# Optimization experiments

Measured on AMD Instinct MI355X. Metric: run time of the kernel, lower is better.

The kernel has to match this reference:

```python
import jax, jax.numpy as jnp
import numpy as np

B, S_IMG, S_TXT, D, H, HD = 1, 4096, 512, 3072, 24, 128
EPS = 1e-5
SCALE = 1.0 / np.sqrt(HD)


def _linear(x, W, b=None):
    # torch nn.Linear: y = x @ W.T + b, W is [out, in]
    y = jnp.einsum('bsd,od->bso', x, W)
    return y if b is None else y + b


def _rmsnorm(x, w):
    # over last dim (head_dim), torch nn.RMSNorm with affine weight
    var = jnp.mean(jnp.square(x), axis=-1, keepdims=True)
    return x * jax.lax.rsqrt(var + EPS) * w


def _rope(x, cos, sin):
    # x: [B, S, H, D]; cos/sin: [S, D]; interleaved-pair rotation
    xr = x.reshape(*x.shape[:-1], HD // 2, 2)
    x_real, x_imag = xr[..., 0], xr[..., 1]
    x_rot = jnp.stack([-x_imag, x_real], axis=-1).reshape(x.shape)
    return x * cos[None, :, None, :] + x_rot * sin[None, :, None, :]


def setup_inputs() -> dict:
    key = jax.random.key(0)
    ks = jax.random.split(key, 24)
    s = 0.02
    inp = {
        'hidden_states': jax.random.normal(ks[0], (B, S_IMG, D), jnp.float32),
        'encoder_hidden_states': jax.random.normal(ks[1], (B, S_TXT, D), jnp.float32),
        'rope_cos': jax.random.uniform(ks[2], (S_IMG + S_TXT, HD), jnp.float32),
        'rope_sin': jax.random.uniform(ks[3], (S_IMG + S_TXT, HD), jnp.float32),
        # image-stream qkv (bias=False)
        'Wq': jax.random.normal(ks[4], (D, D), jnp.float32) * s,
        'Wk': jax.random.normal(ks[5], (D, D), jnp.float32) * s,
        'Wv': jax.random.normal(ks[6], (D, D), jnp.float32) * s,
        # text-stream qkv (bias=True)
        'Waq': jax.random.normal(ks[7], (D, D), jnp.float32) * s,
        'baq': jnp.zeros((D,), jnp.float32),
        'Wak': jax.random.normal(ks[8], (D, D), jnp.float32) * s,
        'bak': jnp.zeros((D,), jnp.float32),
        'Wav': jax.random.normal(ks[9], (D, D), jnp.float32) * s,
        'bav': jnp.zeros((D,), jnp.float32),
        # output projections (bias=True)
        'Wo': jax.random.normal(ks[10], (D, D), jnp.float32) * s,
        'bo': jnp.zeros((D,), jnp.float32),
        'Wao': jax.random.normal(ks[11], (D, D), jnp.float32) * s,
        'bao': jnp.zeros((D,), jnp.float32),
        # RMSNorm weights on head_dim
        'wq_norm': jnp.ones((HD,), jnp.float32),
        'wk_norm': jnp.ones((HD,), jnp.float32),
        'waq_norm': jnp.ones((HD,), jnp.float32),
        'wak_norm': jnp.ones((HD,), jnp.float32),
    }
    return inp


def reference(hidden_states, encoder_hidden_states, rope_cos, rope_sin,
              Wq, Wk, Wv, Waq, baq, Wak, bak, Wav, bav,
              Wo, bo, Wao, bao, wq_norm, wk_norm, waq_norm, wak_norm):
    # image-stream qkv -> [B, S_img, H, HD]
    q = _linear(hidden_states, Wq).reshape(B, S_IMG, H, HD)
    k = _linear(hidden_states, Wk).reshape(B, S_IMG, H, HD)
    v = _linear(hidden_states, Wv).reshape(B, S_IMG, H, HD)
    q = _rmsnorm(q, wq_norm)
    k = _rmsnorm(k, wk_norm)
    # text-stream qkv -> [B, S_txt, H, HD]
    eq = _linear(encoder_hidden_states, Waq, baq).reshape(B, S_TXT, H, HD)
    ek = _linear(encoder_hidden_states, Wak, bak).reshape(B, S_TXT, H, HD)
    ev = _linear(encoder_hidden_states, Wav, bav).reshape(B, S_TXT, H, HD)
    eq = _rmsnorm(eq, waq_norm)
    ek = _rmsnorm(ek, wak_norm)
    # concat [encoder, image] along sequence
    q = jnp.concatenate([eq, q], axis=1)  # [B, S_total, H, HD]
    k = jnp.concatenate([ek, k], axis=1)
    v = jnp.concatenate([ev, v], axis=1)
    # RoPE on joint sequence
    q = _rope(q, rope_cos, rope_sin)
    k = _rope(k, rope_cos, rope_sin)
    # SDPA over joint sequence
    scores = jnp.einsum('bqhd,bkhd->bhqk', q, k) * SCALE
    probs = jax.nn.softmax(scores, axis=-1)
    out = jnp.einsum('bhqk,bkhd->bqhd', probs, v)  # [B, S_total, H, HD]
    out = out.reshape(B, S_IMG + S_TXT, D)
    enc_out = _linear(out[:, :S_TXT], Wao, bao)
    img_out = _linear(out[:, S_TXT:], Wo, bo)
    return (img_out, enc_out)
```

## Files before the change

kernel.cpp:

```cpp
#include <hip/hip_runtime.h>

typedef __bf16 bf16_t;
typedef __bf16 bf16x8 __attribute__((ext_vector_type(8)));
typedef float  f32x4  __attribute__((ext_vector_type(4)));

#define S_IMG 4096
#define S_TXT 512
#define S_TOT 4608
#define DMODEL 3072
#define NH 24
#define HD 128

__device__ __forceinline__ void load_lds16(const void* g, void* l) {
  __builtin_amdgcn_global_load_lds(
      (const __attribute__((address_space(1))) void*)g,
      (__attribute__((address_space(3))) void*)l, 16, 0, 0);
}

#define BARRIER() do { asm volatile("" ::: "memory");                          \
                       __builtin_amdgcn_s_barrier();                           \
                       asm volatile("" ::: "memory"); } while (0)

__global__ __launch_bounds__(256) void f2b_kernel(const float* __restrict__ in,
                                                  bf16_t* __restrict__ out, int n) {
  int i = (blockIdx.x * 256 + threadIdx.x) * 4;
  if (i >= n) return;
  float4 v = *(const float4*)(in + i);
  union { bf16_t b[4]; uint2 u; } pk;
  pk.b[0] = (bf16_t)v.x; pk.b[1] = (bf16_t)v.y;
  pk.b[2] = (bf16_t)v.z; pk.b[3] = (bf16_t)v.w;
  *(uint2*)(out + i) = pk.u;
}

__global__ __launch_bounds__(256) void f2b2_kernel(
    const float* __restrict__ in0, bf16_t* __restrict__ out0,
    const float* __restrict__ in1, bf16_t* __restrict__ out1, int nb) {
  int b = blockIdx.x;
  const float* in = (b < nb) ? in0 : in1;
  bf16_t* out = (b < nb) ? out0 : out1;
  int i = (((b < nb) ? b : b - nb) * 256 + threadIdx.x) * 4;
  float4 v = *(const float4*)(in + i);
  union { bf16_t b[4]; uint2 u; } pk;
  pk.b[0] = (bf16_t)v.x; pk.b[1] = (bf16_t)v.y;
  pk.b[2] = (bf16_t)v.z; pk.b[3] = (bf16_t)v.w;
  *(uint2*)(out + i) = pk.u;
}

template <typename OT>
__global__ __launch_bounds__(512, 2) void gemm256(
    const bf16_t* __restrict__ A0, const bf16_t* __restrict__ B0,
    OT* __restrict__ C0, const float* __restrict__ bias0, int mt0,
    const bf16_t* __restrict__ A1, const bf16_t* __restrict__ B1,
    OT* __restrict__ C1, const float* __restrict__ bias1, int swzq)
{
  const int NT = DMODEL / 64;
  __shared__ bf16_t As[2][2][256 * 32];
  __shared__ bf16_t Bs[2][2][256 * 32];

  int bid = blockIdx.x;
  int t = (bid & 7) * swzq + (bid >> 3);
  int nb0 = mt0 * 12;
  const bf16_t* A; const bf16_t* B; OT* C; const float* bias;
  if (t < nb0) { A = A0; B = B0; C = C0; bias = bias0; }
  else { t -= nb0; A = A1; B = B1; C = C1; bias = bias1; }
  int bx = t % 12, by = t / 12;

  int tid = threadIdx.x;
  int lane = tid & 63, wid = tid >> 6;
  int l15 = lane & 15, lg = lane >> 4;
  int wm = wid >> 2, wn = wid & 3;
  int sx = (lg ^ ((l15 >> 1) & 3)) * 8;

  const bf16_t* Ag = A + (size_t)by * 256 * DMODEL;
  const bf16_t* Bg = B + (size_t)bx * 256 * DMODEL;

  int ur0 = tid >> 2;
  int uc0 = ((tid & 3) ^ ((tid >> 3) & 3)) * 8;

  auto stage = [&](int ht) {
    int T = ht >> 2, sl = ht & 3, kh = sl >> 1;
    const bf16_t* G = (sl & 1) ? Bg : Ag;
    bf16_t* L = (sl & 1) ? &Bs[T & 1][kh][0] : &As[T & 1][kh][0];
    int kbase = T * 64 + kh * 32;
    #pragma unroll
    for (int j = 0; j < 2; j++) {
      int r = j * 128 + ur0;
      load_lds16(G + (size_t)r * DMODEL + kbase + uc0,
                 (char*)L + (size_t)(j * 512 + tid) * 16);
    }
  };

  f32x4 acc[8][4];
  f32x4 zero = {0.f, 0.f, 0.f, 0.f};
  #pragma unroll
  for (int m = 0; m < 8; m++)
    #pragma unroll
    for (int n = 0; n < 4; n++) acc[m][n] = zero;

  stage(0); stage(1); stage(2); stage(3); stage(4); stage(5);
  asm volatile("s_waitcnt vmcnt(8)" ::: "memory");
  BARRIER();

  for (int T = 0; T < NT; ++T) {
    int cur = T & 1;
    const bf16_t* A0s = &As[cur][0][0];
    const bf16_t* A1s = &As[cur][1][0];
    const bf16_t* B0s = &Bs[cur][0][0];
    const bf16_t* B1s = &Bs[cur][1][0];
    bf16x8 af[4], bfr[4];

    #pragma unroll
    for (int n = 0; n < 4; n++)
      bfr[n] = *(const bf16x8*)(B0s + (wn * 64 + n * 16 + l15) * 32 + sx);
    #pragma unroll
    for (int m = 0; m < 4; m++)
      af[m] = *(const bf16x8*)(A0s + (wm * 128 + m * 16 + l15) * 32 + sx);
    if (T + 1 < NT) stage(4 * T + 6);
    BARRIER();
    __builtin_amdgcn_s_setprio(1);
    #pragma unroll
    for (int m = 0; m < 4; m++)
      #pragma unroll
      for (int n = 0; n < 4; n++)
        acc[m][n] = __builtin_amdgcn_mfma_f32_16x16x32_bf16(af[m], bfr[n], acc[m][n], 0, 0, 0);
    __builtin_amdgcn_s_setprio(0);
    BARRIER();

    #pragma unroll
    for (int m = 0; m < 4; m++)
      af[m] = *(const bf16x8*)(A0s + (wm * 128 + 64 + m * 16 + l15) * 32 + sx);
    if (T + 1 < NT) stage(4 * T + 7);
    BARRIER();
    __builtin_amdgcn_s_setprio(1);
    #pragma unroll
    for (int m = 0; m < 4; m++)
      #pragma unroll
      for (int n = 0; n < 4; n++)
        acc[4 + m][n] = __builtin_amdgcn_mfma_f32_16x16x32_bf16(af[m], bfr[n], acc[4 + m][n], 0, 0, 0);
    __builtin_amdgcn_s_setprio(0);
    if (T < NT - 1) asm volatile("s_waitcnt vmcnt(8)" ::: "memory");
    else            asm volatile("s_waitcnt vmcnt(0)" ::: "memory");
    BARRIER();

    #pragma unroll
    for (int n = 0; n < 4; n++)
      bfr[n] = *(const bf16x8*)(B1s + (wn * 64 + n * 16 + l15) * 32 + sx);
    #pragma unroll
    for (int m = 0; m < 4; m++)
      af[m] = *(const bf16x8*)(A1s + (wm * 128 + m * 16 + l15) * 32 + sx);
    if (T + 2 < NT) stage(4 * T + 8);
    BARRIER();
    __builtin_amdgcn_s_setprio(1);
    #pragma unroll
    for (int m = 0; m < 4; m++)
      #pragma unroll
      for (int n = 0; n < 4; n++)
        acc[m][n] = __builtin_amdgcn_mfma_f32_16x16x32_bf16(af[m], bfr[n], acc[m][n], 0, 0, 0);
    __builtin_amdgcn_s_setprio(0);
    BARRIER();

    #pragma unroll
    for (int m = 0; m < 4; m++)
      af[m] = *(const bf16x8*)(A1s + (wm * 128 + 64 + m * 16 + l15) * 32 + sx);
    if (T + 2 < NT) stage(4 * T + 9);
    BARRIER();
    __builtin_amdgcn_s_setprio(1);
    #pragma unroll
    for (int m = 0; m < 4; m++)
      #pragma unroll
      for (int n = 0; n < 4; n++)
        acc[4 + m][n] = __builtin_amdgcn_mfma_f32_16x16x32_bf16(af[m], bfr[n], acc[4 + m][n], 0, 0, 0);
    __builtin_amdgcn_s_setprio(0);
    if (T < NT - 2)       asm volatile("s_waitcnt vmcnt(8)" ::: "memory");
    else if (T == NT - 2) asm volatile("s_waitcnt vmcnt(4)" ::: "memory");
    BARRIER();
  }

  size_t row0 = (size_t)by * 256 + wm * 128;
  int col0 = bx * 256 + wn * 64;
  #pragma unroll
  for (int n = 0; n < 4; n++) {
    int col = col0 + n * 16 + l15;
    float bv = bias ? bias[col] : 0.f;
    #pragma unroll
    for (int m = 0; m < 8; m++) {
      #pragma unroll
      for (int r = 0; r < 4; r++) {
        size_t row = row0 + m * 16 + lg * 4 + r;
        C[row * DMODEL + col] = (OT)(acc[m][n][r] + bv);
      }
    }
  }
}

__global__ __launch_bounds__(256) void qk_post(
    const bf16_t* __restrict__ qbuf, const bf16_t* __restrict__ kbuf,
    const float* __restrict__ cosb, const float* __restrict__ sinb,
    const float* __restrict__ wqn, const float* __restrict__ wkn,
    const float* __restrict__ waqn, const float* __restrict__ wakn,
    bf16_t* __restrict__ Qh, bf16_t* __restrict__ Kh)
{
  int gw = blockIdx.x * 4 + (threadIdx.x >> 6);
  int lane = threadIdx.x & 63;
  int s = gw / NH, h = gw - (gw / NH) * NH;
  if (s >= S_TOT) return;
  int d0 = lane * 2;
  const bf16_t* qp = qbuf + (size_t)s * DMODEL + h * HD + d0;
  const bf16_t* kp = kbuf + (size_t)s * DMODEL + h * HD + d0;
  float q0 = (float)qp[0], q1 = (float)qp[1];
  float k0 = (float)kp[0], k1 = (float)kp[1];
  float sq = q0 * q0 + q1 * q1, sk = k0 * k0 + k1 * k1;
  #pragma unroll
  for (int m = 1; m < 64; m <<= 1) { sq += __shfl_xor(sq, m); sk += __shfl_xor(sk, m); }
  float rq = rsqrtf(sq * (1.f / HD) + 1e-5f);
  float rk = rsqrtf(sk * (1.f / HD) + 1e-5f);
  const float* qn = (s < S_TXT) ? waqn : wqn;
  const float* kn = (s < S_TXT) ? wakn : wkn;
  q0 *= rq * qn[d0]; q1 *= rq * qn[d0 + 1];
  k0 *= rk * kn[d0]; k1 *= rk * kn[d0 + 1];
  float c0 = cosb[s * HD + d0], c1 = cosb[s * HD + d0 + 1];
  float s0 = sinb[s * HD + d0], s1 = sinb[s * HD + d0 + 1];
  const float SCALE = 0.1275174319942397f;
  float oq0 = (q0 * c0 - q1 * s0) * SCALE;
  float oq1 = (q1 * c1 + q0 * s1) * SCALE;
  float ok0 = k0 * c0 - k1 * s0;
  float ok1 = k1 * c1 + k0 * s1;
  size_t ob = ((size_t)h * S_TOT + s) * HD + d0;
  union { bf16_t b[2]; unsigned int u; } pq, pk;
  pq.b[0] = (bf16_t)oq0; pq.b[1] = (bf16_t)oq1;
  pk.b[0] = (bf16_t)ok0; pk.b[1] = (bf16_t)ok1;
  *(unsigned int*)(Qh + ob) = pq.u;
  *(unsigned int*)(Kh + ob) = pk.u;
}

__global__ __launch_bounds__(256) void v_trans(const bf16_t* __restrict__ vbuf,
                                               bf16_t* __restrict__ Vt) {
  __shared__ bf16_t tile[64 * 130];
  int h = blockIdx.y, s0 = blockIdx.x * 64;
  int tid = threadIdx.x;
  #pragma unroll
  for (int i = 0; i < 16; i++) {
    int idx = tid + i * 256;
    int sr = idx >> 6, dp = idx & 63;
    unsigned int u = *(const unsigned int*)(vbuf + (size_t)(s0 + sr) * DMODEL + h * HD + dp * 2);
    *(unsigned int*)&tile[sr * 130 + dp * 2] = u;
  }
  __syncthreads();
  #pragma unroll
  for (int i = 0; i < 16; i++) {
    int idx = tid + i * 256;
    int d = idx >> 5, scp = idx & 31;
    union { bf16_t b[2]; unsigned int u; } pk;
    pk.b[0] = tile[(scp * 2) * 130 + d];
    pk.b[1] = tile[(scp * 2 + 1) * 130 + d];
    *(unsigned int*)(Vt + ((size_t)h * HD + d) * S_TOT + s0 + scp * 2) = pk.u;
  }
}

__global__ __launch_bounds__(256, 2) void attn_kernel(
    const bf16_t* __restrict__ Qh, const bf16_t* __restrict__ Kh,
    const bf16_t* __restrict__ Vt, bf16_t* __restrict__ O)
{
  int bid = blockIdx.x;
  int orig = (bid & 7) * 108 + (bid >> 3);
  int h = orig / 36;
  int q0 = (orig % 36) * 128;

  int tid = threadIdx.x, w = tid >> 6, lane = tid & 63;
  int l15 = lane & 15, lg = lane >> 4;
  int sw = (l15 & 7) << 4;

  __shared__ bf16_t Ks[2][64 * 128];
  __shared__ bf16_t Vs[2][128 * 64];
  __shared__ bf16_t Ps[4][32 * 64];

  const bf16_t* Kbase = Kh + (size_t)h * S_TOT * HD;
  const bf16_t* Vbase = Vt + (size_t)h * HD * S_TOT;
  bf16_t* Pw = &Ps[w][0];

  bf16x8 qf[2][4];
  #pragma unroll
  for (int qh = 0; qh < 2; qh++) {
    const bf16_t* Qrow = Qh + ((size_t)h * S_TOT + q0 + w * 32 + qh * 16 + l15) * HD + lg * 8;
    #pragma unroll
    for (int dc = 0; dc < 4; dc++) qf[qh][dc] = *(const bf16x8*)(Qrow + dc * 32);
  }

  f32x4 o[2][8];
  f32x4 zero = {0.f, 0.f, 0.f, 0.f};
  #pragma unroll
  for (int qh = 0; qh < 2; qh++)
    #pragma unroll
    for (int i = 0; i < 8; i++) o[qh][i] = zero;
  float m0 = -1e30f, m1 = -1e30f, l0 = 0.f, l1 = 0.f;

#define STAGE(buf, kt) do {                                                    \
    _Pragma("unroll")                                                          \
    for (int i_ = 0; i_ < 4; i_++) {                    \
      int Lb = (tid + i_ * 256) * 16; int row = Lb >> 8, cb = Lb & 255;        \
      int sb = cb ^ ((row & 7) << 4);                                          \
      load_lds16(Kbase + (size_t)((kt) + row) * HD + (sb >> 1),                \
                 (char*)Ks[buf] + Lb);                                         \
    }                                                                          \
    _Pragma("unroll")                                                          \
    for (int i_ = 0; i_ < 4; i_++) {                   \
      int Lb = (tid + i_ * 256) * 16; int row = Lb >> 7, cb = Lb & 127;        \
      int sb = cb ^ ((row & 7) << 4);                                          \
      load_lds16(Vbase + (size_t)row * S_TOT + (kt) + (sb >> 1),               \
                 (char*)Vs[buf] + Lb);                                         \
    }                                                                          \
  } while (0)

#define BODY(CUR) do {                                                         \
    f32x4 sacc[2][4];                                                          \
    _Pragma("unroll")                                                          \
    for (int qh = 0; qh < 2; qh++)                                             \
      _Pragma("unroll")                                                        \
      for (int c = 0; c < 4; c++) sacc[qh][c] = zero;                          \
    const char* Kc = (const char*)Ks[CUR];                                     \
    _Pragma("unroll")                                                          \
    for (int c = 0; c < 4; c++) {                                              \
      int row = c * 16 + l15;                                                  \
      int rs = (row & 7) << 4;                                                 \
      const char* kr = Kc + row * 256;                                         \
      _Pragma("unroll")                                                        \
      for (int dc = 0; dc < 4; dc++) {                                         \
        bf16x8 kf = *(const bf16x8*)(kr + ((dc * 64 + lg * 16) ^ rs));         \
        sacc[0][c] = __builtin_amdgcn_mfma_f32_16x16x32_bf16(kf, qf[0][dc], sacc[0][c], 0, 0, 0); \
        sacc[1][c] = __builtin_amdgcn_mfma_f32_16x16x32_bf16(kf, qf[1][dc], sacc[1][c], 0, 0, 0); \
      }                                                                        \
    }                                                                          \
    float px0 = sacc[0][0][0], px1 = sacc[1][0][0];                            \
    _Pragma("unroll")                                                          \
    for (int c = 0; c < 4; c++)                                                \
      _Pragma("unroll")                                                        \
      for (int r = 0; r < 4; r++) {                                            \
        px0 = fmaxf(px0, sacc[0][c][r]);                                       \
        px1 = fmaxf(px1, sacc[1][c][r]);                                       \
      }                                                                        \
    px0 = fmaxf(px0, __shfl_xor(px0, 16)); px0 = fmaxf(px0, __shfl_xor(px0, 32)); \
    px1 = fmaxf(px1, __shfl_xor(px1, 16)); px1 = fmaxf(px1, __shfl_xor(px1, 32)); \
    bool need = (px0 > m0 + 8.f) || (px1 > m1 + 8.f);                          \
    if (__any(need)) {                                                         \
      float mn0 = fmaxf(m0, px0), mn1 = fmaxf(m1, px1);                        \
      float a0 = exp2f(m0 - mn0), a1 = exp2f(m1 - mn1);                        \
      m0 = mn0; m1 = mn1; l0 *= a0; l1 *= a1;                                  \
      _Pragma("unroll")                                                        \
      for (int r = 0; r < 4; r++) {                                            \
        float f0 = __shfl(a0, lg * 4 + r);                                     \
        float f1 = __shfl(a1, lg * 4 + r);                                     \
        _Pragma("unroll")                                                      \
        for (int dn = 0; dn < 8; dn++) { o[0][dn][r] *= f0; o[1][dn][r] *= f1; } \
      }                                                                        \
    }                                                                          \
    _Pragma("unroll")                                                          \
    for (int qh = 0; qh < 2; qh++) {                                           \
      float m = qh ? m1 : m0;                                                  \
      float rsum = 0.f;                                                        \
      char* Prow = (char*)Pw + (qh * 16 + l15) * 128;                          \
      _Pragma("unroll")                                                        \
      for (int c = 0; c < 4; c++) {                                            \
        union { bf16_t b[4]; uint2 u; } pk;                                    \
        _Pragma("unroll")                                                      \
        for (int r = 0; r < 4; r++) {                                          \
          float p = exp2f(sacc[qh][c][r] - m);                                 \
          rsum += p;                                                           \
          pk.b[r] = (bf16_t)p;                                                 \
        }                                                                      \
        *(uint2*)(Prow + ((c * 32 + lg * 8) ^ sw)) = pk.u;                     \
      }                                                                        \
      rsum += __shfl_xor(rsum, 16);                                            \
      rsum += __shfl_xor(rsum, 32);                                            \
      if (qh) l1 += rsum; else l0 += rsum;                                     \
    }                                                                          \
    bf16x8 pf[2][2];                                                           \
    _Pragma("unroll")                                                          \
    for (int qh = 0; qh < 2; qh++) {                                           \
      const char* Prow = (const char*)Pw + (qh * 16 + l15) * 128;              \
      _Pragma("unroll")                                                        \
      for (int kc = 0; kc < 2; kc++)                                           \
        pf[qh][kc] = *(const bf16x8*)(Prow + ((kc * 64 + lg * 16) ^ sw));      \
    }                                                                          \
    const char* Vc = (const char*)Vs[CUR];                                     \
    _Pragma("unroll")                                                          \
    for (int dn = 0; dn < 8; dn++) {                                           \
      int row = dn * 16 + l15;                                                 \
      int rs2 = (row & 7) << 4;                                                \
      const char* vr = Vc + row * 128;                                         \
      bf16x8 vf0 = *(const bf16x8*)(vr + ((lg * 16) ^ rs2));                   \
      bf16x8 vf1 = *(const bf16x8*)(vr + ((64 + lg * 16) ^ rs2));              \
      o[0][dn] = __builtin_amdgcn_mfma_f32_16x16x32_bf16(pf[0][0], vf0, o[0][dn], 0, 0, 0); \
      o[0][dn] = __builtin_amdgcn_mfma_f32_16x16x32_bf16(pf[0][1], vf1, o[0][dn], 0, 0, 0); \
      o[1][dn] = __builtin_amdgcn_mfma_f32_16x16x32_bf16(pf[1][0], vf0, o[1][dn], 0, 0, 0); \
      o[1][dn] = __builtin_amdgcn_mfma_f32_16x16x32_bf16(pf[1][1], vf1, o[1][dn], 0, 0, 0); \
    }                                                                          \
  } while (0)

  STAGE(0, 0);
  __syncthreads();

  const int NT = S_TOT / 64;
  for (int tt = 0; tt < NT; tt += 2) {
    STAGE(1, (tt + 1) * 64);
    BODY(0);
    __syncthreads();
    if (tt + 2 < NT) STAGE(0, (tt + 2) * 64);
    BODY(1);
    __syncthreads();
  }
#undef BODY
#undef STAGE

  #pragma unroll
  for (int qh = 0; qh < 2; qh++) {
    #pragma unroll
    for (int r = 0; r < 4; r++) {
      float lv = __shfl(qh ? l1 : l0, lg * 4 + r);
      float inv = 1.f / lv;
      size_t srow = (size_t)q0 + w * 32 + qh * 16 + lg * 4 + r;
      #pragma unroll
      for (int dn = 0; dn < 8; dn++)
        O[srow * DMODEL + h * HD + dn * 16 + l15] = (bf16_t)(o[qh][dn][r] * inv);
    }
  }
}

extern "C" void kernel_launch(void* const* d_in, const int* in_sizes, int n_in,
                              void* d_out, int out_size, void* d_ws, size_t ws_size,
                              hipStream_t stream) {
  const float* hidden = (const float*)d_in[0];
  const float* enc    = (const float*)d_in[1];
  const float* ropec  = (const float*)d_in[2];
  const float* ropes  = (const float*)d_in[3];
  const float* Wq  = (const float*)d_in[4];
  const float* Wk  = (const float*)d_in[5];
  const float* Wv  = (const float*)d_in[6];
  const float* Waq = (const float*)d_in[7];
  const float* baq = (const float*)d_in[8];
  const float* Wak = (const float*)d_in[9];
  const float* bak = (const float*)d_in[10];
  const float* Wav = (const float*)d_in[11];
  const float* bav = (const float*)d_in[12];
  const float* Wo  = (const float*)d_in[13];
  const float* bo  = (const float*)d_in[14];
  const float* Wao = (const float*)d_in[15];
  const float* bao = (const float*)d_in[16];
  const float* wqn = (const float*)d_in[17];
  const float* wkn = (const float*)d_in[18];
  const float* waqn = (const float*)d_in[19];
  const float* wakn = (const float*)d_in[20];

  const size_t WSZ = (size_t)DMODEL * DMODEL;
  const size_t SEQSZ = (size_t)S_TOT * DMODEL;
  if (ws_size < (2 * WSZ + 6 * SEQSZ) * sizeof(bf16_t)) return;

  bf16_t* s0   = (bf16_t*)d_ws;
  bf16_t* s1   = s0 + WSZ;
  bf16_t* xbi  = s1 + WSZ;
  bf16_t* xbt  = xbi + (size_t)S_IMG * DMODEL;
  bf16_t* qbuf = xbi + SEQSZ;
  bf16_t* kbuf = qbuf + SEQSZ;
  bf16_t* vbuf = kbuf + SEQSZ;
  bf16_t* Kh   = vbuf + SEQSZ;
  bf16_t* Vh   = Kh + SEQSZ;
  bf16_t* Qh   = xbi;
  bf16_t* attn_o = qbuf;
  float* outf = (float*)d_out;

  f2b_kernel<<<S_IMG * DMODEL / 1024, 256, 0, stream>>>(hidden, xbi, S_IMG * DMODEL);
  f2b_kernel<<<S_TXT * DMODEL / 1024, 256, 0, stream>>>(enc, xbt, S_TXT * DMODEL);

  const int WB = (int)(WSZ / 1024);
  f2b2_kernel<<<2 * WB, 256, 0, stream>>>(Wq, s0, Waq, s1, WB);
  gemm256<bf16_t><<<216, 512, 0, stream>>>(
      xbi, s0, qbuf + (size_t)S_TXT * DMODEL, nullptr, 16,
      xbt, s1, qbuf, baq, 27);
  f2b2_kernel<<<2 * WB, 256, 0, stream>>>(Wk, s0, Wak, s1, WB);
  gemm256<bf16_t><<<216, 512, 0, stream>>>(
      xbi, s0, kbuf + (size_t)S_TXT * DMODEL, nullptr, 16,
      xbt, s1, kbuf, bak, 27);
  f2b2_kernel<<<2 * WB, 256, 0, stream>>>(Wv, s0, Wav, s1, WB);
  gemm256<bf16_t><<<216, 512, 0, stream>>>(
      xbi, s0, vbuf + (size_t)S_TXT * DMODEL, nullptr, 16,
      xbt, s1, vbuf, bav, 27);

  qk_post<<<S_TOT * NH / 4, 256, 0, stream>>>(qbuf, kbuf, ropec, ropes,
                                              wqn, wkn, waqn, wakn, Qh, Kh);
  v_trans<<<dim3(S_TOT / 64, NH), 256, 0, stream>>>(vbuf, Vh);

  attn_kernel<<<36 * 24, 256, 0, stream>>>(Qh, Kh, Vh, attn_o);

  f2b2_kernel<<<2 * WB, 256, 0, stream>>>(Wo, s0, Wao, s1, WB);
  gemm256<float><<<216, 512, 0, stream>>>(
      attn_o + (size_t)S_TXT * DMODEL, s0, outf, bo, 16,
      attn_o, s1, outf + (size_t)S_IMG * DMODEL, bao, 27);
}
```

Baseline: 968.5 us.

## Fuse Q/K/V projections into one GEMM launch and pipeline attention K/V loads

Converts all three QKV weight pairs to bf16 up front, placing them in scratch regions (the Kh buffer and the output buffer), and runs a single 648-block GEMM that computes Q, K and V together by treating the weights as a wide N dimension. The output column block picks which matrix to write. Text-stream biases move out of the GEMM and into qk_post and v_trans, with V's bias now added after bf16 rounding. The attention loop is reworked to keep two K/V tiles in flight, using explicit vmcnt waits and raw barriers in place of __syncthreads, and raises wave priority around the MFMA blocks. These changes aim to cut launch count and tail effects and to overlap global loads with compute, at the cost of reusing buffers that the later code must not still need.

```diff
diff --git a/kernel.cpp b/kernel.cpp
--- a/kernel.cpp
+++ b/kernel.cpp
@@ -51,7 +51,8 @@
     const bf16_t* __restrict__ A0, const bf16_t* __restrict__ B0,
     OT* __restrict__ C0, const float* __restrict__ bias0, int mt0,
     const bf16_t* __restrict__ A1, const bf16_t* __restrict__ B1,
-    OT* __restrict__ C1, const float* __restrict__ bias1, int swzq)
+    OT* __restrict__ C1, const float* __restrict__ bias1,
+    int nbt, size_t matStride, int swzq)
 {
   const int NT = DMODEL / 64;
   __shared__ bf16_t As[2][2][256 * 32];
@@ -59,11 +60,12 @@
 
   int bid = blockIdx.x;
   int t = (bid & 7) * swzq + (bid >> 3);
-  int nb0 = mt0 * 12;
+  int nb0 = mt0 * nbt;
   const bf16_t* A; const bf16_t* B; OT* C; const float* bias;
   if (t < nb0) { A = A0; B = B0; C = C0; bias = bias0; }
   else { t -= nb0; A = A1; B = B1; C = C1; bias = bias1; }
-  int bx = t % 12, by = t / 12;
+  int bx = t % nbt, by = t / nbt;
+  int mat = bx / 12;
 
   int tid = threadIdx.x;
   int lane = tid & 63, wid = tid >> 6;
@@ -176,8 +178,9 @@
     BARRIER();
   }
 
+  OT* Cm = C + (size_t)mat * matStride;
   size_t row0 = (size_t)by * 256 + wm * 128;
-  int col0 = bx * 256 + wn * 64;
+  int col0 = (bx % 12) * 256 + wn * 64;
   #pragma unroll
   for (int n = 0; n < 4; n++) {
     int col = col0 + n * 16 + l15;
@@ -187,7 +190,7 @@
       #pragma unroll
       for (int r = 0; r < 4; r++) {
         size_t row = row0 + m * 16 + lg * 4 + r;
-        C[row * DMODEL + col] = (OT)(acc[m][n][r] + bv);
+        Cm[row * DMODEL + col] = (OT)(acc[m][n][r] + bv);
       }
     }
   }
@@ -198,6 +201,7 @@
     const float* __restrict__ cosb, const float* __restrict__ sinb,
     const float* __restrict__ wqn, const float* __restrict__ wkn,
     const float* __restrict__ waqn, const float* __restrict__ wakn,
+    const float* __restrict__ baq, const float* __restrict__ bak,
     bf16_t* __restrict__ Qh, bf16_t* __restrict__ Kh)
 {
   int gw = blockIdx.x * 4 + (threadIdx.x >> 6);
@@ -209,6 +213,10 @@
   const bf16_t* kp = kbuf + (size_t)s * DMODEL + h * HD + d0;
   float q0 = (float)qp[0], q1 = (float)qp[1];
   float k0 = (float)kp[0], k1 = (float)kp[1];
+  if (s < S_TXT) {
+    q0 += baq[h * HD + d0]; q1 += baq[h * HD + d0 + 1];
+    k0 += bak[h * HD + d0]; k1 += bak[h * HD + d0 + 1];
+  }
   float sq = q0 * q0 + q1 * q1, sk = k0 * k0 + k1 * k1;
   #pragma unroll
   for (int m = 1; m < 64; m <<= 1) { sq += __shfl_xor(sq, m); sk += __shfl_xor(sk, m); }
@@ -234,16 +242,23 @@
 }
 
 __global__ __launch_bounds__(256) void v_trans(const bf16_t* __restrict__ vbuf,
+                                               const float* __restrict__ bav,
                                                bf16_t* __restrict__ Vt) {
   __shared__ bf16_t tile[64 * 130];
   int h = blockIdx.y, s0 = blockIdx.x * 64;
   int tid = threadIdx.x;
+  bool txt = (s0 < S_TXT);
   #pragma unroll
   for (int i = 0; i < 16; i++) {
     int idx = tid + i * 256;
     int sr = idx >> 6, dp = idx & 63;
-    unsigned int u = *(const unsigned int*)(vbuf + (size_t)(s0 + sr) * DMODEL + h * HD + dp * 2);
-    *(unsigned int*)&tile[sr * 130 + dp * 2] = u;
+    union { bf16_t b[2]; unsigned int u; } pk;
+    pk.u = *(const unsigned int*)(vbuf + (size_t)(s0 + sr) * DMODEL + h * HD + dp * 2);
+    if (txt) {
+      pk.b[0] = (bf16_t)((float)pk.b[0] + bav[h * HD + dp * 2]);
+      pk.b[1] = (bf16_t)((float)pk.b[1] + bav[h * HD + dp * 2 + 1]);
+    }
+    *(unsigned int*)&tile[sr * 130 + dp * 2] = pk.u;
   }
   __syncthreads();
   #pragma unroll
@@ -318,6 +333,7 @@
       _Pragma("unroll")                                                        \
       for (int c = 0; c < 4; c++) sacc[qh][c] = zero;                          \
     const char* Kc = (const char*)Ks[CUR];                                     \
+    __builtin_amdgcn_s_setprio(1);                                             \
     _Pragma("unroll")                                                          \
     for (int c = 0; c < 4; c++) {                                              \
       int row = c * 16 + l15;                                                  \
@@ -330,6 +346,7 @@
         sacc[1][c] = __builtin_amdgcn_mfma_f32_16x16x32_bf16(kf, qf[1][dc], sacc[1][c], 0, 0, 0); \
       }                                                                        \
     }                                                                          \
+    __builtin_amdgcn_s_setprio(0);                                             \
     float px0 = sacc[0][0][0], px1 = sacc[1][0][0];                            \
     _Pragma("unroll")                                                          \
     for (int c = 0; c < 4; c++)                                                \
@@ -382,6 +399,7 @@
         pf[qh][kc] = *(const bf16x8*)(Prow + ((kc * 64 + lg * 16) ^ sw));      \
     }                                                                          \
     const char* Vc = (const char*)Vs[CUR];                                     \
+    __builtin_amdgcn_s_setprio(1);                                             \
     _Pragma("unroll")                                                          \
     for (int dn = 0; dn < 8; dn++) {                                           \
       int row = dn * 16 + l15;                                                 \
@@ -394,19 +412,25 @@
       o[1][dn] = __builtin_amdgcn_mfma_f32_16x16x32_bf16(pf[1][0], vf0, o[1][dn], 0, 0, 0); \
       o[1][dn] = __builtin_amdgcn_mfma_f32_16x16x32_bf16(pf[1][1], vf1, o[1][dn], 0, 0, 0); \
     }                                                                          \
+    __builtin_amdgcn_s_setprio(0);                                             \
   } while (0)
 
   STAGE(0, 0);
-  __syncthreads();
+  STAGE(1, 64);
 
   const int NT = S_TOT / 64;
   for (int tt = 0; tt < NT; tt += 2) {
-    STAGE(1, (tt + 1) * 64);
+    asm volatile("s_waitcnt vmcnt(8)" ::: "memory");
+    BARRIER();
     BODY(0);
-    __syncthreads();
+    BARRIER();
     if (tt + 2 < NT) STAGE(0, (tt + 2) * 64);
+    if (tt + 2 < NT) asm volatile("s_waitcnt vmcnt(8)" ::: "memory");
+    else             asm volatile("s_waitcnt vmcnt(0)" ::: "memory");
+    BARRIER();
     BODY(1);
-    __syncthreads();
+    BARRIER();
+    if (tt + 3 < NT) STAGE(1, (tt + 3) * 64);
   }
 #undef BODY
 #undef STAGE
@@ -465,33 +489,30 @@
   bf16_t* Vh   = Kh + SEQSZ;
   bf16_t* Qh   = xbi;
   bf16_t* attn_o = qbuf;
+  bf16_t* wimg = Kh;
+  bf16_t* wtxt = (bf16_t*)d_out;
   float* outf = (float*)d_out;
 
   f2b_kernel<<<S_IMG * DMODEL / 1024, 256, 0, stream>>>(hidden, xbi, S_IMG * DMODEL);
   f2b_kernel<<<S_TXT * DMODEL / 1024, 256, 0, stream>>>(enc, xbt, S_TXT * DMODEL);
 
   const int WB = (int)(WSZ / 1024);
-  f2b2_kernel<<<2 * WB, 256, 0, stream>>>(Wq, s0, Waq, s1, WB);
-  gemm256<bf16_t><<<216, 512, 0, stream>>>(
-      xbi, s0, qbuf + (size_t)S_TXT * DMODEL, nullptr, 16,
-      xbt, s1, qbuf, baq, 27);
-  f2b2_kernel<<<2 * WB, 256, 0, stream>>>(Wk, s0, Wak, s1, WB);
-  gemm256<bf16_t><<<216, 512, 0, stream>>>(
-      xbi, s0, kbuf + (size_t)S_TXT * DMODEL, nullptr, 16,
-      xbt, s1, kbuf, bak, 27);
-  f2b2_kernel<<<2 * WB, 256, 0, stream>>>(Wv, s0, Wav, s1, WB);
-  gemm256<bf16_t><<<216, 512, 0, stream>>>(
-      xbi, s0, vbuf + (size_t)S_TXT * DMODEL, nullptr, 16,
-      xbt, s1, vbuf, bav, 27);
+  f2b2_kernel<<<2 * WB, 256, 0, stream>>>(Wq, wimg,           Waq, wtxt,           WB);
+  f2b2_kernel<<<2 * WB, 256, 0, stream>>>(Wk, wimg + WSZ,     Wak, wtxt + WSZ,     WB);
+  f2b2_kernel<<<2 * WB, 256, 0, stream>>>(Wv, wimg + 2 * WSZ, Wav, wtxt + 2 * WSZ, WB);
+
+  gemm256<bf16_t><<<648, 512, 0, stream>>>(
+      xbi, wimg, qbuf + (size_t)S_TXT * DMODEL, nullptr, 16,
+      xbt, wtxt, qbuf, nullptr, 36, SEQSZ, 81);
 
   qk_post<<<S_TOT * NH / 4, 256, 0, stream>>>(qbuf, kbuf, ropec, ropes,
-                                              wqn, wkn, waqn, wakn, Qh, Kh);
-  v_trans<<<dim3(S_TOT / 64, NH), 256, 0, stream>>>(vbuf, Vh);
+                                              wqn, wkn, waqn, wakn, baq, bak, Qh, Kh);
+  v_trans<<<dim3(S_TOT / 64, NH), 256, 0, stream>>>(vbuf, bav, Vh);
 
   attn_kernel<<<36 * 24, 256, 0, stream>>>(Qh, Kh, Vh, attn_o);
 
   f2b2_kernel<<<2 * WB, 256, 0, stream>>>(Wo, s0, Wao, s1, WB);
   gemm256<float><<<216, 512, 0, stream>>>(
       attn_o + (size_t)S_TXT * DMODEL, s0, outf, bo, 16,
-      attn_o, s1, outf + (size_t)S_IMG * DMODEL, bao, 27);
-}
+      attn_o, s1, outf + (size_t)S_IMG * DMODEL, bao, 12, 0, 27);
+}
```

New measurement: 1.044 ms. 1.08x slower.

## Split attention block across 8 waves with 16 query rows each

Applied to the files above, without the earlier changes.

Doubles the attention block to 512 threads, with each of 8 waves owning 16 query rows instead of each of 4 waves owning 32. K/V tiles are still shared in LDS but staged by twice as many threads, and per-wave register state (Q fragments, output accumulators, softmax stats) is halved. The aim is more wave-level parallelism and latency hiding with lower register pressure. In exchange, each K/V LDS fragment read now feeds half as many MFMAs, so LDS traffic per flop rises and barrier costs are shared by more waves.

```diff
diff --git a/kernel.cpp b/kernel.cpp
--- a/kernel.cpp
+++ b/kernel.cpp
@@ -257,7 +257,7 @@
   }
 }
 
-__global__ __launch_bounds__(256, 2) void attn_kernel(
+__global__ __launch_bounds__(512, 2) void attn_kernel(
     const bf16_t* __restrict__ Qh, const bf16_t* __restrict__ Kh,
     const bf16_t* __restrict__ Vt, bf16_t* __restrict__ O)
 {
@@ -272,39 +272,36 @@
 
   __shared__ bf16_t Ks[2][64 * 128];
   __shared__ bf16_t Vs[2][128 * 64];
-  __shared__ bf16_t Ps[4][32 * 64];
+  __shared__ bf16_t Ps[8][16 * 64];
 
   const bf16_t* Kbase = Kh + (size_t)h * S_TOT * HD;
   const bf16_t* Vbase = Vt + (size_t)h * HD * S_TOT;
   bf16_t* Pw = &Ps[w][0];
 
-  bf16x8 qf[2][4];
-  #pragma unroll
-  for (int qh = 0; qh < 2; qh++) {
-    const bf16_t* Qrow = Qh + ((size_t)h * S_TOT + q0 + w * 32 + qh * 16 + l15) * HD + lg * 8;
-    #pragma unroll
-    for (int dc = 0; dc < 4; dc++) qf[qh][dc] = *(const bf16x8*)(Qrow + dc * 32);
-  }
-
-  f32x4 o[2][8];
+  bf16x8 qf[4];
+  {
+    const bf16_t* Qrow = Qh + ((size_t)h * S_TOT + q0 + w * 16 + l15) * HD + lg * 8;
+    #pragma unroll
+    for (int dc = 0; dc < 4; dc++) qf[dc] = *(const bf16x8*)(Qrow + dc * 32);
+  }
+
+  f32x4 o[8];
   f32x4 zero = {0.f, 0.f, 0.f, 0.f};
   #pragma unroll
-  for (int qh = 0; qh < 2; qh++)
-    #pragma unroll
-    for (int i = 0; i < 8; i++) o[qh][i] = zero;
-  float m0 = -1e30f, m1 = -1e30f, l0 = 0.f, l1 = 0.f;
+  for (int i = 0; i < 8; i++) o[i] = zero;
+  float m0 = -1e30f, l0 = 0.f;
 
 #define STAGE(buf, kt) do {                                                    \
     _Pragma("unroll")                                                          \
-    for (int i_ = 0; i_ < 4; i_++) {                    \
-      int Lb = (tid + i_ * 256) * 16; int row = Lb >> 8, cb = Lb & 255;        \
+    for (int i_ = 0; i_ < 2; i_++) {           \
+      int Lb = (tid + i_ * 512) * 16; int row = Lb >> 8, cb = Lb & 255;        \
       int sb = cb ^ ((row & 7) << 4);                                          \
       load_lds16(Kbase + (size_t)((kt) + row) * HD + (sb >> 1),                \
                  (char*)Ks[buf] + Lb);                                         \
     }                                                                          \
     _Pragma("unroll")                                                          \
-    for (int i_ = 0; i_ < 4; i_++) {                   \
-      int Lb = (tid + i_ * 256) * 16; int row = Lb >> 7, cb = Lb & 127;        \
+    for (int i_ = 0; i_ < 2; i_++) {                   \
+      int Lb = (tid + i_ * 512) * 16; int row = Lb >> 7, cb = Lb & 127;        \
       int sb = cb ^ ((row & 7) << 4);                                          \
       load_lds16(Vbase + (size_t)row * S_TOT + (kt) + (sb >> 1),               \
                  (char*)Vs[buf] + Lb);                                         \
@@ -312,11 +309,8 @@
   } while (0)
 
 #define BODY(CUR) do {                                                         \
-    f32x4 sacc[2][4];                                                          \
-    _Pragma("unroll")                                                          \
-    for (int qh = 0; qh < 2; qh++)                                             \
-      _Pragma("unroll")                                                        \
-      for (int c = 0; c < 4; c++) sacc[qh][c] = zero;                          \
+    f32x4 sacc[4];                                                             \
+    sacc[0] = zero; sacc[1] = zero; sacc[2] = zero; sacc[3] = zero;            \
     const char* Kc = (const char*)Ks[CUR];                                     \
     _Pragma("unroll")                                                          \
     for (int c = 0; c < 4; c++) {                                              \
@@ -326,44 +320,36 @@
       _Pragma("unroll")                                                        \
       for (int dc = 0; dc < 4; dc++) {                                         \
         bf16x8 kf = *(const bf16x8*)(kr + ((dc * 64 + lg * 16) ^ rs));         \
-        sacc[0][c] = __builtin_amdgcn_mfma_f32_16x16x32_bf16(kf, qf[0][dc], sacc[0][c], 0, 0, 0); \
-        sacc[1][c] = __builtin_amdgcn_mfma_f32_16x16x32_bf16(kf, qf[1][dc], sacc[1][c], 0, 0, 0); \
+        sacc[c] = __builtin_amdgcn_mfma_f32_16x16x32_bf16(kf, qf[dc], sacc[c], 0, 0, 0); \
       }                                                                        \
     }                                                                          \
-    float px0 = sacc[0][0][0], px1 = sacc[1][0][0];                            \
+    float px = sacc[0][0];                                                     \
     _Pragma("unroll")                                                          \
     for (int c = 0; c < 4; c++)                                                \
       _Pragma("unroll")                                                        \
-      for (int r = 0; r < 4; r++) {                                            \
-        px0 = fmaxf(px0, sacc[0][c][r]);                                       \
-        px1 = fmaxf(px1, sacc[1][c][r]);                                       \
-      }                                                                        \
-    px0 = fmaxf(px0, __shfl_xor(px0, 16)); px0 = fmaxf(px0, __shfl_xor(px0, 32)); \
-    px1 = fmaxf(px1, __shfl_xor(px1, 16)); px1 = fmaxf(px1, __shfl_xor(px1, 32)); \
-    bool need = (px0 > m0 + 8.f) || (px1 > m1 + 8.f);                          \
-    if (__any(need)) {                                                         \
-      float mn0 = fmaxf(m0, px0), mn1 = fmaxf(m1, px1);                        \
-      float a0 = exp2f(m0 - mn0), a1 = exp2f(m1 - mn1);                        \
-      m0 = mn0; m1 = mn1; l0 *= a0; l1 *= a1;                                  \
+      for (int r = 0; r < 4; r++) px = fmaxf(px, sacc[c][r]);                  \
+    px = fmaxf(px, __shfl_xor(px, 16));                                        \
+    px = fmaxf(px, __shfl_xor(px, 32));                                        \
+    if (__any(px > m0 + 8.f)) {                                                \
+      float mn0 = fmaxf(m0, px);                                               \
+      float a0 = exp2f(m0 - mn0);                                              \
+      m0 = mn0; l0 *= a0;                                                      \
       _Pragma("unroll")                                                        \
       for (int r = 0; r < 4; r++) {                                            \
         float f0 = __shfl(a0, lg * 4 + r);                                     \
-        float f1 = __shfl(a1, lg * 4 + r);                                     \
         _Pragma("unroll")                                                      \
-        for (int dn = 0; dn < 8; dn++) { o[0][dn][r] *= f0; o[1][dn][r] *= f1; } \
+        for (int dn = 0; dn < 8; dn++) o[dn][r] *= f0;                         \
       }                                                                        \
     }                                                                          \
-    _Pragma("unroll")                                                          \
-    for (int qh = 0; qh < 2; qh++) {                                           \
-      float m = qh ? m1 : m0;                                                  \
+    {                                                                          \
       float rsum = 0.f;                                                        \
-      char* Prow = (char*)Pw + (qh * 16 + l15) * 128;                          \
+      char* Prow = (char*)Pw + l15 * 128;                                      \
       _Pragma("unroll")                                                        \
       for (int c = 0; c < 4; c++) {                                            \
         union { bf16_t b[4]; uint2 u; } pk;                                    \
         _Pragma("unroll")                                                      \
         for (int r = 0; r < 4; r++) {                                          \
-          float p = exp2f(sacc[qh][c][r] - m);                                 \
+          float p = exp2f(sacc[c][r] - m0);                                    \
           rsum += p;                                                           \
           pk.b[r] = (bf16_t)p;                                                 \
         }                                                                      \
@@ -371,15 +357,14 @@
       }                                                                        \
       rsum += __shfl_xor(rsum, 16);                                            \
       rsum += __shfl_xor(rsum, 32);                                            \
-      if (qh) l1 += rsum; else l0 += rsum;                                     \
-    }                                                                          \
-    bf16x8 pf[2][2];                                                           \
-    _Pragma("unroll")                                                          \
-    for (int qh = 0; qh < 2; qh++) {                                           \
-      const char* Prow = (const char*)Pw + (qh * 16 + l15) * 128;              \
+      l0 += rsum;                                                              \
+    }                                                                          \
+    bf16x8 pf[2];                                                              \
+    {                                                                          \
+      const char* Prow = (const char*)Pw + l15 * 128;                          \
       _Pragma("unroll")                                                        \
       for (int kc = 0; kc < 2; kc++)                                           \
-        pf[qh][kc] = *(const bf16x8*)(Prow + ((kc * 64 + lg * 16) ^ sw));      \
+        pf[kc] = *(const bf16x8*)(Prow + ((kc * 64 + lg * 16) ^ sw));          \
     }                                                                          \
     const char* Vc = (const char*)Vs[CUR];                                     \
     _Pragma("unroll")                                                          \
@@ -389,10 +374,8 @@
       const char* vr = Vc + row * 128;                                         \
       bf16x8 vf0 = *(const bf16x8*)(vr + ((lg * 16) ^ rs2));                   \
       bf16x8 vf1 = *(const bf16x8*)(vr + ((64 + lg * 16) ^ rs2));              \
-      o[0][dn] = __builtin_amdgcn_mfma_f32_16x16x32_bf16(pf[0][0], vf0, o[0][dn], 0, 0, 0); \
-      o[0][dn] = __builtin_amdgcn_mfma_f32_16x16x32_bf16(pf[0][1], vf1, o[0][dn], 0, 0, 0); \
-      o[1][dn] = __builtin_amdgcn_mfma_f32_16x16x32_bf16(pf[1][0], vf0, o[1][dn], 0, 0, 0); \
-      o[1][dn] = __builtin_amdgcn_mfma_f32_16x16x32_bf16(pf[1][1], vf1, o[1][dn], 0, 0, 0); \
+      o[dn] = __builtin_amdgcn_mfma_f32_16x16x32_bf16(pf[0], vf0, o[dn], 0, 0, 0); \
+      o[dn] = __builtin_amdgcn_mfma_f32_16x16x32_bf16(pf[1], vf1, o[dn], 0, 0, 0); \
     }                                                                          \
   } while (0)
 
@@ -412,16 +395,13 @@
 #undef STAGE
 
   #pragma unroll
-  for (int qh = 0; qh < 2; qh++) {
-    #pragma unroll
-    for (int r = 0; r < 4; r++) {
-      float lv = __shfl(qh ? l1 : l0, lg * 4 + r);
-      float inv = 1.f / lv;
-      size_t srow = (size_t)q0 + w * 32 + qh * 16 + lg * 4 + r;
-      #pragma unroll
-      for (int dn = 0; dn < 8; dn++)
-        O[srow * DMODEL + h * HD + dn * 16 + l15] = (bf16_t)(o[qh][dn][r] * inv);
-    }
+  for (int r = 0; r < 4; r++) {
+    float lv = __shfl(l0, lg * 4 + r);
+    float inv = 1.f / lv;
+    size_t srow = (size_t)q0 + w * 16 + lg * 4 + r;
+    #pragma unroll
+    for (int dn = 0; dn < 8; dn++)
+      O[srow * DMODEL + h * HD + dn * 16 + l15] = (bf16_t)(o[dn][r] * inv);
   }
 }
 
@@ -488,7 +468,7 @@
                                               wqn, wkn, waqn, wakn, Qh, Kh);
   v_trans<<<dim3(S_TOT / 64, NH), 256, 0, stream>>>(vbuf, Vh);
 
-  attn_kernel<<<36 * 24, 256, 0, stream>>>(Qh, Kh, Vh, attn_o);
+  attn_kernel<<<36 * 24, 512, 0, stream>>>(Qh, Kh, Vh, attn_o);
 
   f2b2_kernel<<<2 * WB, 256, 0, stream>>>(Wo, s0, Wao, s1, WB);
   gemm256<float><<<216, 512, 0, stream>>>(
```

Measured after the change: 981.3 us. About the same (+1.3%).

## Grow attention query tile to 192 rows with three 16-row groups per wave

Applied to the files above, without the earlier changes.

The attention kernel now assigns 48 query rows per wave (192 per block) instead of 32, so each K/V tile staged into LDS is reused across more queries and the grid shrinks from 864 to 576 blocks. P staging is reworked to use a single 16-row LDS slot per wave, reused per query group, to keep LDS usage down. This reduces K/V global traffic and barrier count per query but raises register pressure (three accumulator sets of 8 f32x4), which may cause spills or lower occupancy at launch_bounds(256,2). The block count of 576 also changes how evenly work is spread over the CUs.

```diff
diff --git a/kernel.cpp b/kernel.cpp
--- a/kernel.cpp
+++ b/kernel.cpp
@@ -262,9 +262,9 @@
     const bf16_t* __restrict__ Vt, bf16_t* __restrict__ O)
 {
   int bid = blockIdx.x;
-  int orig = (bid & 7) * 108 + (bid >> 3);
-  int h = orig / 36;
-  int q0 = (orig % 36) * 128;
+  int orig = (bid & 7) * 72 + (bid >> 3);
+  int h = orig / 24;
+  int q0 = (orig % 24) * 192;
 
   int tid = threadIdx.x, w = tid >> 6, lane = tid & 63;
   int l15 = lane & 15, lg = lane >> 4;
@@ -272,27 +272,28 @@
 
   __shared__ bf16_t Ks[2][64 * 128];
   __shared__ bf16_t Vs[2][128 * 64];
-  __shared__ bf16_t Ps[4][32 * 64];
+  __shared__ bf16_t Ps[4][16 * 64];
 
   const bf16_t* Kbase = Kh + (size_t)h * S_TOT * HD;
   const bf16_t* Vbase = Vt + (size_t)h * HD * S_TOT;
   bf16_t* Pw = &Ps[w][0];
 
-  bf16x8 qf[2][4];
-  #pragma unroll
-  for (int qh = 0; qh < 2; qh++) {
-    const bf16_t* Qrow = Qh + ((size_t)h * S_TOT + q0 + w * 32 + qh * 16 + l15) * HD + lg * 8;
+  bf16x8 qf[3][4];
+  #pragma unroll
+  for (int qh = 0; qh < 3; qh++) {
+    const bf16_t* Qrow = Qh + ((size_t)h * S_TOT + q0 + w * 48 + qh * 16 + l15) * HD + lg * 8;
     #pragma unroll
     for (int dc = 0; dc < 4; dc++) qf[qh][dc] = *(const bf16x8*)(Qrow + dc * 32);
   }
 
-  f32x4 o[2][8];
+  f32x4 o[3][8];
   f32x4 zero = {0.f, 0.f, 0.f, 0.f};
   #pragma unroll
-  for (int qh = 0; qh < 2; qh++)
+  for (int qh = 0; qh < 3; qh++)
     #pragma unroll
     for (int i = 0; i < 8; i++) o[qh][i] = zero;
-  float m0 = -1e30f, m1 = -1e30f, l0 = 0.f, l1 = 0.f;
+  float m0 = -1e30f, m1 = -1e30f, m2 = -1e30f;
+  float l0 = 0.f, l1 = 0.f, l2 = 0.f;
 
 #define STAGE(buf, kt) do {                                                    \
     _Pragma("unroll")                                                          \
@@ -312,9 +313,9 @@
   } while (0)
 
 #define BODY(CUR) do {                                                         \
-    f32x4 sacc[2][4];                                                          \
-    _Pragma("unroll")                                                          \
-    for (int qh = 0; qh < 2; qh++)                                             \
+    f32x4 sacc[3][4];                                                          \
+    _Pragma("unroll")                                                          \
+    for (int qh = 0; qh < 3; qh++)                                             \
       _Pragma("unroll")                                                        \
       for (int c = 0; c < 4; c++) sacc[qh][c] = zero;                          \
     const char* Kc = (const char*)Ks[CUR];                                     \
@@ -328,36 +329,43 @@
         bf16x8 kf = *(const bf16x8*)(kr + ((dc * 64 + lg * 16) ^ rs));         \
         sacc[0][c] = __builtin_amdgcn_mfma_f32_16x16x32_bf16(kf, qf[0][dc], sacc[0][c], 0, 0, 0); \
         sacc[1][c] = __builtin_amdgcn_mfma_f32_16x16x32_bf16(kf, qf[1][dc], sacc[1][c], 0, 0, 0); \
+        sacc[2][c] = __builtin_amdgcn_mfma_f32_16x16x32_bf16(kf, qf[2][dc], sacc[2][c], 0, 0, 0); \
       }                                                                        \
     }                                                                          \
-    float px0 = sacc[0][0][0], px1 = sacc[1][0][0];                            \
+    float px0 = sacc[0][0][0], px1 = sacc[1][0][0], px2 = sacc[2][0][0];       \
     _Pragma("unroll")                                                          \
     for (int c = 0; c < 4; c++)                                                \
       _Pragma("unroll")                                                        \
       for (int r = 0; r < 4; r++) {                                            \
         px0 = fmaxf(px0, sacc[0][c][r]);                                       \
         px1 = fmaxf(px1, sacc[1][c][r]);                                       \
+        px2 = fmaxf(px2, sacc[2][c][r]);                                       \
       }                                                                        \
     px0 = fmaxf(px0, __shfl_xor(px0, 16)); px0 = fmaxf(px0, __shfl_xor(px0, 32)); \
     px1 = fmaxf(px1, __shfl_xor(px1, 16)); px1 = fmaxf(px1, __shfl_xor(px1, 32)); \
-    bool need = (px0 > m0 + 8.f) || (px1 > m1 + 8.f);                          \
+    px2 = fmaxf(px2, __shfl_xor(px2, 16)); px2 = fmaxf(px2, __shfl_xor(px2, 32)); \
+    bool need = (px0 > m0 + 8.f) || (px1 > m1 + 8.f) || (px2 > m2 + 8.f);      \
     if (__any(need)) {                                                         \
-      float mn0 = fmaxf(m0, px0), mn1 = fmaxf(m1, px1);                        \
-      float a0 = exp2f(m0 - mn0), a1 = exp2f(m1 - mn1);                        \
-      m0 = mn0; m1 = mn1; l0 *= a0; l1 *= a1;                                  \
+      float mn0 = fmaxf(m0, px0), mn1 = fmaxf(m1, px1), mn2 = fmaxf(m2, px2);  \
+      float a0 = exp2f(m0 - mn0), a1 = exp2f(m1 - mn1), a2 = exp2f(m2 - mn2);  \
+      m0 = mn0; m1 = mn1; m2 = mn2; l0 *= a0; l1 *= a1; l2 *= a2;              \
       _Pragma("unroll")                                                        \
       for (int r = 0; r < 4; r++) {                                            \
         float f0 = __shfl(a0, lg * 4 + r);                                     \
         float f1 = __shfl(a1, lg * 4 + r);                                     \
+        float f2 = __shfl(a2, lg * 4 + r);                                     \
         _Pragma("unroll")                                                      \
-        for (int dn = 0; dn < 8; dn++) { o[0][dn][r] *= f0; o[1][dn][r] *= f1; } \
+        for (int dn = 0; dn < 8; dn++) {                                       \
+          o[0][dn][r] *= f0; o[1][dn][r] *= f1; o[2][dn][r] *= f2;             \
+        }                                                                      \
       }                                                                        \
     }                                                                          \
-    _Pragma("unroll")                                                          \
-    for (int qh = 0; qh < 2; qh++) {                                           \
-      float m = qh ? m1 : m0;                                                  \
+    bf16x8 pf[3][2];                                                           \
+    _Pragma("unroll")                                                          \
+    for (int qh = 0; qh < 3; qh++) {                                           \
+      float m = (qh == 0) ? m0 : (qh == 1) ? m1 : m2;                          \
       float rsum = 0.f;                                                        \
-      char* Prow = (char*)Pw + (qh * 16 + l15) * 128;                          \
+      char* Prow = (char*)Pw + l15 * 128;                                      \
       _Pragma("unroll")                                                        \
       for (int c = 0; c < 4; c++) {                                            \
         union { bf16_t b[4]; uint2 u; } pk;                                    \
@@ -371,15 +379,10 @@
       }                                                                        \
       rsum += __shfl_xor(rsum, 16);                                            \
       rsum += __shfl_xor(rsum, 32);                                            \
-      if (qh) l1 += rsum; else l0 += rsum;                                     \
-    }                                                                          \
-    bf16x8 pf[2][2];                                                           \
-    _Pragma("unroll")                                                          \
-    for (int qh = 0; qh < 2; qh++) {                                           \
-      const char* Prow = (const char*)Pw + (qh * 16 + l15) * 128;              \
+      if (qh == 0) l0 += rsum; else if (qh == 1) l1 += rsum; else l2 += rsum;  \
       _Pragma("unroll")                                                        \
       for (int kc = 0; kc < 2; kc++)                                           \
-        pf[qh][kc] = *(const bf16x8*)(Prow + ((kc * 64 + lg * 16) ^ sw));      \
+        pf[qh][kc] = *(const bf16x8*)((const char*)Prow + ((kc * 64 + lg * 16) ^ sw)); \
     }                                                                          \
     const char* Vc = (const char*)Vs[CUR];                                     \
     _Pragma("unroll")                                                          \
@@ -393,6 +396,8 @@
       o[0][dn] = __builtin_amdgcn_mfma_f32_16x16x32_bf16(pf[0][1], vf1, o[0][dn], 0, 0, 0); \
       o[1][dn] = __builtin_amdgcn_mfma_f32_16x16x32_bf16(pf[1][0], vf0, o[1][dn], 0, 0, 0); \
       o[1][dn] = __builtin_amdgcn_mfma_f32_16x16x32_bf16(pf[1][1], vf1, o[1][dn], 0, 0, 0); \
+      o[2][dn] = __builtin_amdgcn_mfma_f32_16x16x32_bf16(pf[2][0], vf0, o[2][dn], 0, 0, 0); \
+      o[2][dn] = __builtin_amdgcn_mfma_f32_16x16x32_bf16(pf[2][1], vf1, o[2][dn], 0, 0, 0); \
     }                                                                          \
   } while (0)
 
@@ -412,12 +417,13 @@
 #undef STAGE
 
   #pragma unroll
-  for (int qh = 0; qh < 2; qh++) {
+  for (int qh = 0; qh < 3; qh++) {
+    float lq = (qh == 0) ? l0 : (qh == 1) ? l1 : l2;
     #pragma unroll
     for (int r = 0; r < 4; r++) {
-      float lv = __shfl(qh ? l1 : l0, lg * 4 + r);
+      float lv = __shfl(lq, lg * 4 + r);
       float inv = 1.f / lv;
-      size_t srow = (size_t)q0 + w * 32 + qh * 16 + lg * 4 + r;
+      size_t srow = (size_t)q0 + w * 48 + qh * 16 + lg * 4 + r;
       #pragma unroll
       for (int dn = 0; dn < 8; dn++)
         O[srow * DMODEL + h * HD + dn * 16 + l15] = (bf16_t)(o[qh][dn][r] * inv);
@@ -488,7 +494,7 @@
                                               wqn, wkn, waqn, wakn, Qh, Kh);
   v_trans<<<dim3(S_TOT / 64, NH), 256, 0, stream>>>(vbuf, Vh);
 
-  attn_kernel<<<36 * 24, 256, 0, stream>>>(Qh, Kh, Vh, attn_o);
+  attn_kernel<<<576, 256, 0, stream>>>(Qh, Kh, Vh, attn_o);
 
   f2b2_kernel<<<2 * WB, 256, 0, stream>>>(Wo, s0, Wao, s1, WB);
   gemm256<float><<<216, 512, 0, stream>>>(
```

After: 1.107 ms. 1.14x slower.
